# Kernel optimization log

Measured on AMD Instinct MI355X. Metric: run time of the kernel, lower is better.

## Reference

```python
import jax, jax.numpy as jnp
import numpy as np

THR = 1.0   # snntorch Leaky default threshold
BETA = 0.9  # leak factor from the module


@jax.custom_vjp
def atan_spike(x):
    # Heaviside forward; ATan surrogate gradient (snntorch default alpha=2):
    # d/dx = 1 / (1 + (pi * x)^2)
    return (x > 0).astype(x.dtype)

def _atan_fwd(x):
    return (x > 0).astype(x.dtype), x

def _atan_bwd(x, g):
    return (g / (1.0 + (jnp.pi * x) ** 2),)

atan_spike.defvjp(_atan_fwd, _atan_bwd)


def setup_inputs() -> dict:
    key = jax.random.key(0)
    k0, k1, k2, k3, k4 = jax.random.split(key, 5)
    B, T, L = 256, 1000, 30  # 24 = L - 7 + 1 matches fc1 in_features 16*24
    out_c = 35
    x = jax.random.normal(k0, (B, T, L), dtype=jnp.float32)
    conv_w = jax.random.normal(k1, (16, 1, 7), dtype=jnp.float32) / np.float32(np.sqrt(7.0))
    conv_b = jax.random.normal(k2, (16,), dtype=jnp.float32) * 0.05
    fc_w = jax.random.normal(k3, (out_c, 16 * 24), dtype=jnp.float32) / np.float32(np.sqrt(384.0))
    fc_b = jax.random.normal(k4, (out_c,), dtype=jnp.float32) * 0.05
    return {"x": x, "conv_w": conv_w, "conv_b": conv_b, "fc_w": fc_w, "fc_b": fc_b}


def reference(x, conv_w, conv_b, fc_w, fc_b):
    B, T, L = x.shape
    # Conv1d has no recurrence -> hoist it out of the time loop, batched over B*T.
    cur1 = jax.lax.conv_general_dilated(
        x.reshape(B * T, 1, L), conv_w, window_strides=(1,), padding="VALID",
        dimension_numbers=("NCH", "OIH", "NCH"),
    ) + conv_b[None, :, None]                      # (B*T, 16, 24)
    Lo = cur1.shape[-1]
    cur1 = cur1.reshape(B, T, 16, Lo).transpose(1, 0, 2, 3)  # (T, B, 16, 24)
    out_c = fc_w.shape[0]

    def step(carry, c1):
        mem1, mem2 = carry
        # LIF1: reset-by-subtraction using detached spike of previous membrane
        r1 = jax.lax.stop_gradient((mem1 > THR).astype(mem1.dtype))
        mem1 = BETA * mem1 + c1 - r1 * THR
        spk1 = atan_spike(mem1 - THR)              # (B, 16, 24)
        c2 = spk1.reshape(B, 16 * Lo) @ fc_w.T + fc_b  # (B, out_c)
        # LIF2
        r2 = jax.lax.stop_gradient((mem2 > THR).astype(mem2.dtype))
        mem2 = BETA * mem2 + c2 - r2 * THR
        return (mem1, mem2), mem2

    init = (jnp.zeros((B, 16, Lo), x.dtype), jnp.zeros((B, out_c), x.dtype))
    _, mem2_rec = jax.lax.scan(step, init, cur1)   # (T, B, out_c)
    return mem2_rec.mean(axis=0)                   # (B, out_c)
```

## Files before the change

### kernel.cpp

```cpp
#include <hip/hip_runtime.h>

typedef _Float16 half8 __attribute__((ext_vector_type(8)));
typedef float f32x4 __attribute__((ext_vector_type(4)));

#define SPH  32
#define NIT  34
#define SPKW 392
#define XSW  32
#define C2W  48
#define TN   1000

__global__ __launch_bounds__(384) void snn_fwd(
    const float* __restrict__ x,
    const float* __restrict__ conv_w,
    const float* __restrict__ conv_b,
    const float* __restrict__ fc_w,
    const float* __restrict__ fc_b,
    float* __restrict__ out)
{
    __shared__ _Float16 spk[2][SPH][SPKW];
    __shared__ float    xs[2][SPH][XSW];
    __shared__ float    c2L[2][SPH][C2W];

    const int tid  = threadIdx.x;
    const int b    = blockIdx.x;
    const int wid  = tid >> 6;
    const int lane = tid & 63;

    const int ct = tid;
    const int c  = ct / 12;
    const int u  = ct % 12;
    float wk[7];
    float cb = 0.f;
    if (wid < 3) {
#pragma unroll
        for (int k = 0; k < 7; ++k) wk[k] = conv_w[c * 7 + k];
        cb = conv_b[c];
    }

    const int m  = wid - 3;
    const int nL = lane & 15;
    const int q  = lane >> 4;
    half8 A[12];
    if (wid >= 3) {
        const int o = m * 16 + nL;
#pragma unroll
        for (int kt = 0; kt < 12; ++kt) {
            half8 a;
#pragma unroll
            for (int j = 0; j < 8; ++j) {
                int K = kt * 32 + q * 8 + j;
                a[j] = (o < 35) ? (_Float16)fc_w[o * 384 + K] : (_Float16)0.f;
            }
            A[kt] = a;
        }
    }
    const float fcb = (wid == 3 && lane < 35) ? fc_b[lane] : 0.f;

    float m10 = 0.f, m11 = 0.f, sp0 = 0.f, sp1 = 0.f;
    float mem2 = 0.f, accO = 0.f;

    const float* xb = x + (size_t)b * (TN * 30);

    if (wid < 3) {
#pragma unroll
        for (int r = 0; r < 5; ++r) {
            int f = ct + 192 * r;
            xs[0][f / 30][f % 30] = xb[f];
        }
    }
    __syncthreads();

#pragma unroll 1
    for (int ph = 0; ph < NIT; ++ph) {
        if (wid < 3) {
            float xr[5];
            const bool stg = (ph <= 30);
            if (stg) {
                const float* src = xb + (ph + 1) * (SPH * 30);
#pragma unroll
                for (int r = 0; r < 5; ++r) {
                    int f = ct + 192 * r;
                    int t = (ph + 1) * SPH + f / 30;
                    xr[r] = (t < TN) ? src[f] : 0.f;
                }
            }
            if (ph < 32) {
                const float* xrow = &xs[ph & 1][0][2 * u];
                _Float16* sdst = &spk[ph & 1][0][2 * ct];
#pragma unroll 4
                for (int s = 0; s < SPH; ++s) {
                    const float2* x2 = (const float2*)(xrow + s * XSW);
                    float2 a0 = x2[0], a1 = x2[1], a2 = x2[2], a3 = x2[3];
                    float c1a = cb, c1b = cb;
                    c1a = fmaf(wk[0], a0.x, c1a);  c1b = fmaf(wk[0], a0.y, c1b);
                    c1a = fmaf(wk[1], a0.y, c1a);  c1b = fmaf(wk[1], a1.x, c1b);
                    c1a = fmaf(wk[2], a1.x, c1a);  c1b = fmaf(wk[2], a1.y, c1b);
                    c1a = fmaf(wk[3], a1.y, c1a);  c1b = fmaf(wk[3], a2.x, c1b);
                    c1a = fmaf(wk[4], a2.x, c1a);  c1b = fmaf(wk[4], a2.y, c1b);
                    c1a = fmaf(wk[5], a2.y, c1a);  c1b = fmaf(wk[5], a3.x, c1b);
                    c1a = fmaf(wk[6], a3.x, c1a);  c1b = fmaf(wk[6], a3.y, c1b);

                    m10 = fmaf(0.9f, m10, c1a - sp0);
                    m11 = fmaf(0.9f, m11, c1b - sp1);
                    sp0 = (m10 > 1.0f) ? 1.0f : 0.0f;
                    sp1 = (m11 > 1.0f) ? 1.0f : 0.0f;
                    unsigned pk = (m10 > 1.0f ? 0x3C00u : 0u) | (m11 > 1.0f ? 0x3C000000u : 0u);
                    *(unsigned*)(sdst + s * SPKW) = pk;
                }
            }
            if (stg) {
                float* dst = &xs[(ph + 1) & 1][0][0];
#pragma unroll
                for (int r = 0; r < 5; ++r) {
                    int f = ct + 192 * r;
                    dst[(f / 30) * XSW + (f % 30)] = xr[r];
                }
            }
        } else {
            if (ph >= 1 && ph <= 32) {
                const _Float16* sb = &spk[(ph - 1) & 1][0][0];
                half8 B0[12], B1[12];
#pragma unroll
                for (int kt = 0; kt < 12; ++kt) {
                    B0[kt] = *(const half8*)(sb + nL * SPKW + kt * 32 + q * 8);
                    B1[kt] = *(const half8*)(sb + (16 + nL) * SPKW + kt * 32 + q * 8);
                }
                f32x4 acc0 = {0.f, 0.f, 0.f, 0.f};
                f32x4 acc1 = {0.f, 0.f, 0.f, 0.f};
#pragma unroll
                for (int kt = 0; kt < 12; ++kt) {
                    acc0 = __builtin_amdgcn_mfma_f32_16x16x32_f16(A[kt], B0[kt], acc0, 0, 0, 0);
                    acc1 = __builtin_amdgcn_mfma_f32_16x16x32_f16(A[kt], B1[kt], acc1, 0, 0, 0);
                }
                float* cd = &c2L[(ph - 1) & 1][0][0];
                *(f32x4*)(cd + nL * C2W + m * 16 + q * 4)        = acc0;
                *(f32x4*)(cd + (16 + nL) * C2W + m * 16 + q * 4) = acc1;
            }
            if (wid == 3 && lane < 35 && ph >= 2) {
                const float* cs = &c2L[(ph - 2) & 1][0][0];
                const int tb = (ph - 2) * SPH;
#pragma unroll
                for (int s8 = 0; s8 < SPH; s8 += 8) {
                    float v[8];
#pragma unroll
                    for (int j = 0; j < 8; ++j) v[j] = cs[(s8 + j) * C2W + lane] + fcb;
#pragma unroll
                    for (int j = 0; j < 8; ++j) {
                        float r2 = (mem2 > 1.0f) ? 1.0f : 0.0f;
                        mem2 = 0.9f * mem2 + v[j] - r2;
                        if (tb + s8 + j < TN) accO += mem2;
                    }
                }
            }
        }
        __syncthreads();
    }

    if (wid == 3 && lane < 35) out[b * 35 + lane] = accO * (1.0f / (float)TN);
}

extern "C" void kernel_launch(void* const* d_in, const int* in_sizes, int n_in,
                              void* d_out, int out_size, void* d_ws, size_t ws_size,
                              hipStream_t stream) {
    const float* x      = (const float*)d_in[0];
    const float* conv_w = (const float*)d_in[1];
    const float* conv_b = (const float*)d_in[2];
    const float* fc_w   = (const float*)d_in[3];
    const float* fc_b   = (const float*)d_in[4];
    float* out          = (float*)d_out;

    snn_fwd<<<256, 384, 0, stream>>>(x, conv_w, conv_b, fc_w, fc_b, out);
}
```

Baseline: 169.1 us.

## Double time chunk per phase and interleave LIF2 scan with MFMA GEMM

Raises the per-phase time chunk from 32 to 64 steps, halving the number of block-wide barriers and phases. The GEMM warps now process the chunk in two 32-row halves. In each half, warp 3 runs the LIF2 scan on the previous phase's currents, so the scalar scan overlaps with MFMA work instead of trailing it. Shared memory arrays scale with SPH, which raises LDS use and could cap occupancy (launch bounds now say one block per CU) and adds register pressure from the larger staging arrays.

New measurement: 178.7 us. 1.06x slower.

```diff
diff --git a/kernel.cpp b/kernel.cpp
--- a/kernel.cpp
+++ b/kernel.cpp
@@ -3,14 +3,14 @@
 typedef _Float16 half8 __attribute__((ext_vector_type(8)));
 typedef float f32x4 __attribute__((ext_vector_type(4)));
 
-#define SPH  32
-#define NIT  34
+#define SPH  64
+#define NIT  18
 #define SPKW 392
 #define XSW  32
 #define C2W  48
 #define TN   1000
 
-__global__ __launch_bounds__(384) void snn_fwd(
+__global__ __launch_bounds__(384, 1) void snn_fwd(
     const float* __restrict__ x,
     const float* __restrict__ conv_w,
     const float* __restrict__ conv_b,
@@ -64,7 +64,7 @@
 
     if (wid < 3) {
 #pragma unroll
-        for (int r = 0; r < 5; ++r) {
+        for (int r = 0; r < 10; ++r) {
             int f = ct + 192 * r;
             xs[0][f / 30][f % 30] = xb[f];
         }
@@ -74,18 +74,18 @@
 #pragma unroll 1
     for (int ph = 0; ph < NIT; ++ph) {
         if (wid < 3) {
-            float xr[5];
-            const bool stg = (ph <= 30);
+            float xr[10];
+            const bool stg = (ph <= 14);
             if (stg) {
                 const float* src = xb + (ph + 1) * (SPH * 30);
 #pragma unroll
-                for (int r = 0; r < 5; ++r) {
+                for (int r = 0; r < 10; ++r) {
                     int f = ct + 192 * r;
                     int t = (ph + 1) * SPH + f / 30;
                     xr[r] = (t < TN) ? src[f] : 0.f;
                 }
             }
-            if (ph < 32) {
+            if (ph < 16) {
                 const float* xrow = &xs[ph & 1][0][2 * u];
                 _Float16* sdst = &spk[ph & 1][0][2 * ct];
 #pragma unroll 4
@@ -112,44 +112,51 @@
             if (stg) {
                 float* dst = &xs[(ph + 1) & 1][0][0];
 #pragma unroll
-                for (int r = 0; r < 5; ++r) {
+                for (int r = 0; r < 10; ++r) {
                     int f = ct + 192 * r;
                     dst[(f / 30) * XSW + (f % 30)] = xr[r];
                 }
             }
         } else {
-            if (ph >= 1 && ph <= 32) {
-                const _Float16* sb = &spk[(ph - 1) & 1][0][0];
-                half8 B0[12], B1[12];
+            const bool doGemm = (ph >= 1 && ph <= 16);
+            const bool doScan = (wid == 3 && lane < 35 && ph >= 2);
+            const _Float16* sb = &spk[(ph - 1) & 1][0][0];
+            float*          cd = &c2L[(ph - 1) & 1][0][0];
+            const float*    cs = &c2L[ph & 1][0][0];
+
 #pragma unroll
-                for (int kt = 0; kt < 12; ++kt) {
-                    B0[kt] = *(const half8*)(sb + nL * SPKW + kt * 32 + q * 8);
-                    B1[kt] = *(const half8*)(sb + (16 + nL) * SPKW + kt * 32 + q * 8);
+            for (int tb = 0; tb < 2; ++tb) {
+                float v[32];
+                if (doScan) {
+#pragma unroll
+                    for (int j = 0; j < 32; ++j)
+                        v[j] = cs[(tb * 32 + j) * C2W + lane];
                 }
-                f32x4 acc0 = {0.f, 0.f, 0.f, 0.f};
-                f32x4 acc1 = {0.f, 0.f, 0.f, 0.f};
+                if (doGemm) {
+                    const _Float16* sbt = sb + (32 * tb) * SPKW;
+                    half8 B0[12], B1[12];
 #pragma unroll
-                for (int kt = 0; kt < 12; ++kt) {
-                    acc0 = __builtin_amdgcn_mfma_f32_16x16x32_f16(A[kt], B0[kt], acc0, 0, 0, 0);
-                    acc1 = __builtin_amdgcn_mfma_f32_16x16x32_f16(A[kt], B1[kt], acc1, 0, 0, 0);
+                    for (int kt = 0; kt < 12; ++kt) {
+                        B0[kt] = *(const half8*)(sbt + nL * SPKW + kt * 32 + q * 8);
+                        B1[kt] = *(const half8*)(sbt + (16 + nL) * SPKW + kt * 32 + q * 8);
+                    }
+                    f32x4 acc0 = {0.f, 0.f, 0.f, 0.f};
+                    f32x4 acc1 = {0.f, 0.f, 0.f, 0.f};
+#pragma unroll
+                    for (int kt = 0; kt < 12; ++kt) {
+                        acc0 = __builtin_amdgcn_mfma_f32_16x16x32_f16(A[kt], B0[kt], acc0, 0, 0, 0);
+                        acc1 = __builtin_amdgcn_mfma_f32_16x16x32_f16(A[kt], B1[kt], acc1, 0, 0, 0);
+                    }
+                    *(f32x4*)(cd + (32 * tb + nL) * C2W + m * 16 + q * 4)        = acc0;
+                    *(f32x4*)(cd + (32 * tb + 16 + nL) * C2W + m * 16 + q * 4)   = acc1;
                 }
-                float* cd = &c2L[(ph - 1) & 1][0][0];
-                *(f32x4*)(cd + nL * C2W + m * 16 + q * 4)        = acc0;
-                *(f32x4*)(cd + (16 + nL) * C2W + m * 16 + q * 4) = acc1;
-            }
-            if (wid == 3 && lane < 35 && ph >= 2) {
-                const float* cs = &c2L[(ph - 2) & 1][0][0];
-                const int tb = (ph - 2) * SPH;
+                if (doScan) {
+                    const int tb0 = (ph - 2) * SPH + tb * 32;
 #pragma unroll
-                for (int s8 = 0; s8 < SPH; s8 += 8) {
-                    float v[8];
-#pragma unroll
-                    for (int j = 0; j < 8; ++j) v[j] = cs[(s8 + j) * C2W + lane] + fcb;
-#pragma unroll
-                    for (int j = 0; j < 8; ++j) {
+                    for (int j = 0; j < 32; ++j) {
                         float r2 = (mem2 > 1.0f) ? 1.0f : 0.0f;
-                        mem2 = 0.9f * mem2 + v[j] - r2;
-                        if (tb + s8 + j < TN) accO += mem2;
+                        mem2 = 0.9f * mem2 + (v[j] + fcb) - r2;
+                        if (tb0 + j < TN) accO += mem2;
                     }
                 }
             }
```

## Read conv inputs directly from global memory and hoist LIF2 loads before MFMA

Applied to the files above, without the earlier changes.

Drops the shared-memory double-buffered staging of x. Conv warps now load their float2 windows straight from global memory, bounds-checked per timestep. The LIF2 scan's 32 LDS loads are issued before the MFMA block so their latency can overlap with the matrix work. Launch bounds now request one block per SM, which frees more registers. The trade-off is that global-load latency now sits directly in the serial membrane recurrence with no prefetch, and the reads are unaligned and overlapping.

Result: slower. 423.1 us (+150.3%).

```diff
diff --git a/kernel.cpp b/kernel.cpp
--- a/kernel.cpp
+++ b/kernel.cpp
@@ -6,11 +6,10 @@
 #define SPH  32
 #define NIT  34
 #define SPKW 392
-#define XSW  32
 #define C2W  48
 #define TN   1000
 
-__global__ __launch_bounds__(384) void snn_fwd(
+__global__ __launch_bounds__(384, 1) void snn_fwd(
     const float* __restrict__ x,
     const float* __restrict__ conv_w,
     const float* __restrict__ conv_b,
@@ -19,7 +18,6 @@
     float* __restrict__ out)
 {
     __shared__ _Float16 spk[2][SPH][SPKW];
-    __shared__ float    xs[2][SPH][XSW];
     __shared__ float    c2L[2][SPH][C2W];
 
     const int tid  = threadIdx.x;
@@ -62,36 +60,24 @@
 
     const float* xb = x + (size_t)b * (TN * 30);
 
-    if (wid < 3) {
-#pragma unroll
-        for (int r = 0; r < 5; ++r) {
-            int f = ct + 192 * r;
-            xs[0][f / 30][f % 30] = xb[f];
-        }
-    }
     __syncthreads();
 
 #pragma unroll 1
     for (int ph = 0; ph < NIT; ++ph) {
         if (wid < 3) {
-            float xr[5];
-            const bool stg = (ph <= 30);
-            if (stg) {
-                const float* src = xb + (ph + 1) * (SPH * 30);
-#pragma unroll
-                for (int r = 0; r < 5; ++r) {
-                    int f = ct + 192 * r;
-                    int t = (ph + 1) * SPH + f / 30;
-                    xr[r] = (t < TN) ? src[f] : 0.f;
-                }
-            }
             if (ph < 32) {
-                const float* xrow = &xs[ph & 1][0][2 * u];
+                const int t0 = ph * SPH;
+                const float* xrow = xb + (size_t)t0 * 30 + 2 * u;
                 _Float16* sdst = &spk[ph & 1][0][2 * ct];
 #pragma unroll 4
                 for (int s = 0; s < SPH; ++s) {
-                    const float2* x2 = (const float2*)(xrow + s * XSW);
-                    float2 a0 = x2[0], a1 = x2[1], a2 = x2[2], a3 = x2[3];
+                    float2 a0, a1, a2, a3;
+                    if (t0 + s < TN) {
+                        const float2* x2 = (const float2*)(xrow + s * 30);
+                        a0 = x2[0]; a1 = x2[1]; a2 = x2[2]; a3 = x2[3];
+                    } else {
+                        a0 = a1 = a2 = a3 = make_float2(0.f, 0.f);
+                    }
                     float c1a = cb, c1b = cb;
                     c1a = fmaf(wk[0], a0.x, c1a);  c1b = fmaf(wk[0], a0.y, c1b);
                     c1a = fmaf(wk[1], a0.y, c1a);  c1b = fmaf(wk[1], a1.x, c1b);
@@ -109,15 +95,14 @@
                     *(unsigned*)(sdst + s * SPKW) = pk;
                 }
             }
-            if (stg) {
-                float* dst = &xs[(ph + 1) & 1][0][0];
+        } else {
+            const bool doScan = (wid == 3 && lane < 35 && ph >= 2);
+            float v[SPH];
+            if (doScan) {
+                const float* cs = &c2L[(ph - 2) & 1][0][0];
 #pragma unroll
-                for (int r = 0; r < 5; ++r) {
-                    int f = ct + 192 * r;
-                    dst[(f / 30) * XSW + (f % 30)] = xr[r];
-                }
+                for (int j = 0; j < SPH; ++j) v[j] = cs[j * C2W + lane];
             }
-        } else {
             if (ph >= 1 && ph <= 32) {
                 const _Float16* sb = &spk[(ph - 1) & 1][0][0];
                 half8 B0[12], B1[12];
@@ -137,20 +122,13 @@
                 *(f32x4*)(cd + nL * C2W + m * 16 + q * 4)        = acc0;
                 *(f32x4*)(cd + (16 + nL) * C2W + m * 16 + q * 4) = acc1;
             }
-            if (wid == 3 && lane < 35 && ph >= 2) {
-                const float* cs = &c2L[(ph - 2) & 1][0][0];
+            if (doScan) {
                 const int tb = (ph - 2) * SPH;
 #pragma unroll
-                for (int s8 = 0; s8 < SPH; s8 += 8) {
-                    float v[8];
-#pragma unroll
-                    for (int j = 0; j < 8; ++j) v[j] = cs[(s8 + j) * C2W + lane] + fcb;
-#pragma unroll
-                    for (int j = 0; j < 8; ++j) {
-                        float r2 = (mem2 > 1.0f) ? 1.0f : 0.0f;
-                        mem2 = 0.9f * mem2 + v[j] - r2;
-                        if (tb + s8 + j < TN) accO += mem2;
-                    }
+                for (int j = 0; j < SPH; ++j) {
+                    float r2 = (mem2 > 1.0f) ? 1.0f : 0.0f;
+                    mem2 = 0.9f * mem2 + (v[j] + fcb) - r2;
+                    if (tb + j < TN) accO += mem2;
                 }
             }
         }
```

## Give conv threads two channels each and prefetch LIF2 inputs before MFMA

Applied to the files above, without the earlier changes.

The convolution and LIF1 stage now runs on 96 threads instead of 192. Each thread handles channels c and c+8, giving four independent membrane chains per step for more instruction-level parallelism and leaving part of the conv waves idle. The LIF2 scan wave now loads all 32 c2 values from LDS before running its MFMA block, so LDS latency overlaps with the matrix work. Launch bounds now declare one block per SM. The risks are longer per-thread serial work in the conv stage and higher register pressure from the 32-value prefetch buffer.

After: 228.0 us. 1.35x slower.

```diff
diff --git a/kernel.cpp b/kernel.cpp
--- a/kernel.cpp
+++ b/kernel.cpp
@@ -10,7 +10,7 @@
 #define C2W  48
 #define TN   1000
 
-__global__ __launch_bounds__(384) void snn_fwd(
+__global__ __launch_bounds__(384, 1) void snn_fwd(
     const float* __restrict__ x,
     const float* __restrict__ conv_w,
     const float* __restrict__ conv_b,
@@ -27,15 +27,18 @@
     const int wid  = tid >> 6;
     const int lane = tid & 63;
 
-    const int ct = tid;
-    const int c  = ct / 12;
-    const int u  = ct % 12;
-    float wk[7];
-    float cb = 0.f;
-    if (wid < 3) {
+    const int c  = tid / 12;
+    const int u  = tid % 12;
+    float wkA[7], wkB[7];
+    float cbA = 0.f, cbB = 0.f;
+    if (tid < 96) {
 #pragma unroll
-        for (int k = 0; k < 7; ++k) wk[k] = conv_w[c * 7 + k];
-        cb = conv_b[c];
+        for (int k = 0; k < 7; ++k) {
+            wkA[k] = conv_w[c * 7 + k];
+            wkB[k] = conv_w[(c + 8) * 7 + k];
+        }
+        cbA = conv_b[c];
+        cbB = conv_b[c + 8];
     }
 
     const int m  = wid - 3;
@@ -57,7 +60,8 @@
     }
     const float fcb = (wid == 3 && lane < 35) ? fc_b[lane] : 0.f;
 
-    float m10 = 0.f, m11 = 0.f, sp0 = 0.f, sp1 = 0.f;
+    float m1A0 = 0.f, m1A1 = 0.f, m1B0 = 0.f, m1B1 = 0.f;
+    float spA0 = 0.f, spA1 = 0.f, spB0 = 0.f, spB1 = 0.f;
     float mem2 = 0.f, accO = 0.f;
 
     const float* xb = x + (size_t)b * (TN * 30);
@@ -65,7 +69,7 @@
     if (wid < 3) {
 #pragma unroll
         for (int r = 0; r < 5; ++r) {
-            int f = ct + 192 * r;
+            int f = tid + 192 * r;
             xs[0][f / 30][f % 30] = xb[f];
         }
     }
@@ -80,44 +84,67 @@
                 const float* src = xb + (ph + 1) * (SPH * 30);
 #pragma unroll
                 for (int r = 0; r < 5; ++r) {
-                    int f = ct + 192 * r;
+                    int f = tid + 192 * r;
                     int t = (ph + 1) * SPH + f / 30;
                     xr[r] = (t < TN) ? src[f] : 0.f;
                 }
             }
-            if (ph < 32) {
+            if (tid < 96 && ph < 32) {
                 const float* xrow = &xs[ph & 1][0][2 * u];
-                _Float16* sdst = &spk[ph & 1][0][2 * ct];
+                _Float16* sbase = &spk[ph & 1][0][0];
+                const int colA = c * 24 + 2 * u;
+                const int colB = (c + 8) * 24 + 2 * u;
 #pragma unroll 4
                 for (int s = 0; s < SPH; ++s) {
                     const float2* x2 = (const float2*)(xrow + s * XSW);
                     float2 a0 = x2[0], a1 = x2[1], a2 = x2[2], a3 = x2[3];
-                    float c1a = cb, c1b = cb;
-                    c1a = fmaf(wk[0], a0.x, c1a);  c1b = fmaf(wk[0], a0.y, c1b);
-                    c1a = fmaf(wk[1], a0.y, c1a);  c1b = fmaf(wk[1], a1.x, c1b);
-                    c1a = fmaf(wk[2], a1.x, c1a);  c1b = fmaf(wk[2], a1.y, c1b);
-                    c1a = fmaf(wk[3], a1.y, c1a);  c1b = fmaf(wk[3], a2.x, c1b);
-                    c1a = fmaf(wk[4], a2.x, c1a);  c1b = fmaf(wk[4], a2.y, c1b);
-                    c1a = fmaf(wk[5], a2.y, c1a);  c1b = fmaf(wk[5], a3.x, c1b);
-                    c1a = fmaf(wk[6], a3.x, c1a);  c1b = fmaf(wk[6], a3.y, c1b);
+                    float cA0 = cbA, cA1 = cbA, cB0 = cbB, cB1 = cbB;
+                    cA0 = fmaf(wkA[0], a0.x, cA0);  cA1 = fmaf(wkA[0], a0.y, cA1);
+                    cB0 = fmaf(wkB[0], a0.x, cB0);  cB1 = fmaf(wkB[0], a0.y, cB1);
+                    cA0 = fmaf(wkA[1], a0.y, cA0);  cA1 = fmaf(wkA[1], a1.x, cA1);
+                    cB0 = fmaf(wkB[1], a0.y, cB0);  cB1 = fmaf(wkB[1], a1.x, cB1);
+                    cA0 = fmaf(wkA[2], a1.x, cA0);  cA1 = fmaf(wkA[2], a1.y, cA1);
+                    cB0 = fmaf(wkB[2], a1.x, cB0);  cB1 = fmaf(wkB[2], a1.y, cB1);
+                    cA0 = fmaf(wkA[3], a1.y, cA0);  cA1 = fmaf(wkA[3], a2.x, cA1);
+                    cB0 = fmaf(wkB[3], a1.y, cB0);  cB1 = fmaf(wkB[3], a2.x, cB1);
+                    cA0 = fmaf(wkA[4], a2.x, cA0);  cA1 = fmaf(wkA[4], a2.y, cA1);
+                    cB0 = fmaf(wkB[4], a2.x, cB0);  cB1 = fmaf(wkB[4], a2.y, cB1);
+                    cA0 = fmaf(wkA[5], a2.y, cA0);  cA1 = fmaf(wkA[5], a3.x, cA1);
+                    cB0 = fmaf(wkB[5], a2.y, cB0);  cB1 = fmaf(wkB[5], a3.x, cB1);
+                    cA0 = fmaf(wkA[6], a3.x, cA0);  cA1 = fmaf(wkA[6], a3.y, cA1);
+                    cB0 = fmaf(wkB[6], a3.x, cB0);  cB1 = fmaf(wkB[6], a3.y, cB1);
 
-                    m10 = fmaf(0.9f, m10, c1a - sp0);
-                    m11 = fmaf(0.9f, m11, c1b - sp1);
-                    sp0 = (m10 > 1.0f) ? 1.0f : 0.0f;
-                    sp1 = (m11 > 1.0f) ? 1.0f : 0.0f;
-                    unsigned pk = (m10 > 1.0f ? 0x3C00u : 0u) | (m11 > 1.0f ? 0x3C000000u : 0u);
-                    *(unsigned*)(sdst + s * SPKW) = pk;
+                    m1A0 = fmaf(0.9f, m1A0, cA0 - spA0);
+                    m1A1 = fmaf(0.9f, m1A1, cA1 - spA1);
+                    m1B0 = fmaf(0.9f, m1B0, cB0 - spB0);
+                    m1B1 = fmaf(0.9f, m1B1, cB1 - spB1);
+                    spA0 = (m1A0 > 1.0f) ? 1.0f : 0.0f;
+                    spA1 = (m1A1 > 1.0f) ? 1.0f : 0.0f;
+                    spB0 = (m1B0 > 1.0f) ? 1.0f : 0.0f;
+                    spB1 = (m1B1 > 1.0f) ? 1.0f : 0.0f;
+                    unsigned pkA = (m1A0 > 1.0f ? 0x3C00u : 0u) | (m1A1 > 1.0f ? 0x3C000000u : 0u);
+                    unsigned pkB = (m1B0 > 1.0f ? 0x3C00u : 0u) | (m1B1 > 1.0f ? 0x3C000000u : 0u);
+                    _Float16* srow = sbase + s * SPKW;
+                    *(unsigned*)(srow + colA) = pkA;
+                    *(unsigned*)(srow + colB) = pkB;
                 }
             }
             if (stg) {
                 float* dst = &xs[(ph + 1) & 1][0][0];
 #pragma unroll
                 for (int r = 0; r < 5; ++r) {
-                    int f = ct + 192 * r;
+                    int f = tid + 192 * r;
                     dst[(f / 30) * XSW + (f % 30)] = xr[r];
                 }
             }
         } else {
+            const bool doScan = (wid == 3 && lane < 35 && ph >= 2);
+            float v[SPH];
+            if (doScan) {
+                const float* cs = &c2L[(ph - 2) & 1][0][0];
+#pragma unroll
+                for (int j = 0; j < SPH; ++j) v[j] = cs[j * C2W + lane];
+            }
             if (ph >= 1 && ph <= 32) {
                 const _Float16* sb = &spk[(ph - 1) & 1][0][0];
                 half8 B0[12], B1[12];
@@ -137,20 +164,13 @@
                 *(f32x4*)(cd + nL * C2W + m * 16 + q * 4)        = acc0;
                 *(f32x4*)(cd + (16 + nL) * C2W + m * 16 + q * 4) = acc1;
             }
-            if (wid == 3 && lane < 35 && ph >= 2) {
-                const float* cs = &c2L[(ph - 2) & 1][0][0];
+            if (doScan) {
                 const int tb = (ph - 2) * SPH;
 #pragma unroll
-                for (int s8 = 0; s8 < SPH; s8 += 8) {
-                    float v[8];
-#pragma unroll
-                    for (int j = 0; j < 8; ++j) v[j] = cs[(s8 + j) * C2W + lane] + fcb;
-#pragma unroll
-                    for (int j = 0; j < 8; ++j) {
-                        float r2 = (mem2 > 1.0f) ? 1.0f : 0.0f;
-                        mem2 = 0.9f * mem2 + v[j] - r2;
-                        if (tb + s8 + j < TN) accO += mem2;
-                    }
+                for (int j = 0; j < SPH; ++j) {
+                    float r2 = (mem2 > 1.0f) ? 1.0f : 0.0f;
+                    mem2 = 0.9f * mem2 + (v[j] + fcb) - r2;
+                    if (tb + j < TN) accO += mem2;
                 }
             }
         }
```
